# Optimization experiments

Hardware: AMD Instinct MI355X
Metric: run time of the kernel (lower is better)

The kernel has to match this reference:

```python
import jax, jax.numpy as jnp
import numpy as np

N_NODES = 100000
N_EDGES = 1600000
IN_DIM, HID_DIM, OUT_DIM = 128, 64, 16
BN_EPS = 1e-5


def sage_conv(x, edge_index, W_l, b_l, W_r):
    # PyG SAGEConv (aggr='mean'): out = lin_l(mean_j x_j) + lin_r(x_i)
    src, dst = edge_index[0], edge_index[1]
    msgs = x[src]                                   # [E, F] gather
    sums = jax.ops.segment_sum(msgs, dst, num_segments=N_NODES)      # [N, F]
    cnt = jax.ops.segment_sum(jnp.ones((src.shape[0],), x.dtype), dst,
                              num_segments=N_NODES)                  # [N]
    agg = sums / jnp.maximum(cnt, 1.0)[:, None]     # mean; 0 for isolated nodes
    return agg @ W_l.T + b_l + x @ W_r.T


def batchnorm(x, gamma, beta):
    # BatchNorm1d in training mode: normalize over the node (batch) axis
    mean = jnp.mean(x, axis=0)
    var = jnp.var(x, axis=0)
    return (x - mean) * jax.lax.rsqrt(var + BN_EPS) * gamma + beta


def setup_inputs() -> dict:
    key = jax.random.key(0)
    ks = jax.random.split(key, 8)
    x = jax.random.normal(ks[0], (N_NODES, IN_DIM), dtype=jnp.float32)
    edge_index = jax.random.randint(ks[1], (2, N_EDGES), 0, N_NODES)
    s1 = 1.0 / np.sqrt(IN_DIM)
    s2 = 1.0 / np.sqrt(HID_DIM)
    return {
        "x": x,
        "edge_index": edge_index,
        "W1_l": jax.random.uniform(ks[2], (HID_DIM, IN_DIM), minval=-s1, maxval=s1),
        "b1": jnp.zeros((HID_DIM,), jnp.float32),
        "W1_r": jax.random.uniform(ks[3], (HID_DIM, IN_DIM), minval=-s1, maxval=s1),
        "bn_gamma": jnp.ones((HID_DIM,), jnp.float32),
        "bn_beta": jnp.zeros((HID_DIM,), jnp.float32),
        "W2_l": jax.random.uniform(ks[4], (OUT_DIM, HID_DIM), minval=-s2, maxval=s2),
        "b2": jnp.zeros((OUT_DIM,), jnp.float32),
        "W2_r": jax.random.uniform(ks[5], (OUT_DIM, HID_DIM), minval=-s2, maxval=s2),
    }


def reference(x, edge_index, W1_l, b1, W1_r, bn_gamma, bn_beta, W2_l, b2, W2_r):
    h = sage_conv(x, edge_index, W1_l, b1, W1_r)
    h = jax.nn.relu(batchnorm(h, bn_gamma, bn_beta))
    return sage_conv(h, edge_index, W2_l, b2, W2_r)
```

## Files before the change

kernel.cpp:

```cpp
#include <hip/hip_runtime.h>

#define NN 100000
#define NE 1600000
#define NPB 128
#define NBK 782
#define EPB 16384
#define NPART 98
#define NTILES 1563
#define CAP 4096

#define OFF_H      0
#define OFF_YL     6400000
#define OFF_YR     9600000
#define OFF_EBUF   12800000
#define OFF_HIST   14400000
#define OFF_BSTART 14500000
#define OFF_BCURP  14500800
#define OFF_BCNTP  14513312
#define OFF_BNACC  14525824

typedef __attribute__((ext_vector_type(8))) short bf16x8;
typedef __attribute__((ext_vector_type(4))) float f32x4;

__device__ __forceinline__ ushort f2bf(float f) {
  unsigned u = __float_as_uint(f);
  u += 0x7fffu + ((u >> 16) & 1);
  return (ushort)(u >> 16);
}
#define BFLO(u) __uint_as_float(((u) & 0xffffu) << 16)
#define BFHI(u) __uint_as_float((u) & 0xffff0000u)

__global__ __launch_bounds__(1024) void k_bcnt2(const int* __restrict__ ei,
                                                int* __restrict__ bcntp) {
  __shared__ int cnt[NBK];
  const int tid = threadIdx.x;
  for (int i = tid; i < NBK; i += 1024) cnt[i] = 0;
  __syncthreads();
  const int per = (NE + gridDim.x - 1) / gridDim.x;
  int e0 = blockIdx.x * per;
  int e1 = min(e0 + per, NE);
  for (int e = e0 + tid; e < e1; e += 1024)
    atomicAdd(&cnt[ei[NE + e] >> 7], 1);
  __syncthreads();
  for (int b = tid; b < NBK; b += 1024)
    if (cnt[b]) atomicAdd(&bcntp[b * 16], cnt[b]);
}

__global__ __launch_bounds__(1024) void k_bprep(const int* __restrict__ bcntp,
                                                int* __restrict__ bstart,
                                                int* __restrict__ bcurp) {
  __shared__ int sd[1024];
  int t = threadIdx.x;
  int v = (t < NBK) ? bcntp[t * 16] : 0;
  sd[t] = v;
  __syncthreads();
  for (int off = 1; off < 1024; off <<= 1) {
    int u = (t >= off) ? sd[t - off] : 0;
    __syncthreads();
    sd[t] += u;
    __syncthreads();
  }
  if (t < NBK) { int s = sd[t] - v; bstart[t] = s; bcurp[t * 16] = s; }
  if (t == 0) bstart[NBK] = NE;
}

__global__ __launch_bounds__(512) void k_pg(const int* __restrict__ ei,
                                            int* __restrict__ bcurp,
                                            int* __restrict__ ebuf,
                                            const float* __restrict__ x,
                                            const float* __restrict__ W1l,
                                            const float* __restrict__ W1r,
                                            ushort* __restrict__ yl,
                                            ushort* __restrict__ yr) {
  __shared__ ushort smem[64 * 136 + 128 * 136];
  const int tid = threadIdx.x;

  if (blockIdx.x < NPART) {
    int* cnt = (int*)smem;
    int* gstart = cnt + NBK;
    int* cur = gstart + NBK;
    int e0 = blockIdx.x * EPB;
    int e1 = min(e0 + EPB, NE);
    for (int i = tid; i < NBK; i += 512) cnt[i] = 0;
    __syncthreads();
    for (int e = e0 + tid; e < e1; e += 512)
      atomicAdd(&cnt[ei[NE + e] >> 7], 1);
    __syncthreads();
    for (int b = tid; b < NBK; b += 512) {
      int c = cnt[b];
      gstart[b] = c ? atomicAdd(&bcurp[b * 16], c) : 0;
      cur[b] = 0;
    }
    __syncthreads();
    for (int e = e0 + tid; e < e1; e += 512) {
      int s = ei[e], t = ei[NE + e];
      int b = t >> 7;
      int r = atomicAdd(&cur[b], 1);
      ebuf[gstart[b] + r] = (s << 7) | (t & 127);
    }
    return;
  }

  ushort* xs = smem;
  ushort* wss = smem + 64 * 136;
  const int n0 = (blockIdx.x - NPART) * 64;

  for (int i = tid; i < 64 * 32; i += 512) {
    int r = i >> 5, c = i & 31;
    int n = n0 + r;
    float4 v = (n < NN) ? *(const float4*)&x[(size_t)n * 128 + c * 4]
                        : make_float4(0.f, 0.f, 0.f, 0.f);
    *(ushort4*)&xs[r * 136 + c * 4] = make_ushort4(f2bf(v.x), f2bf(v.y), f2bf(v.z), f2bf(v.w));
  }
  for (int i = tid; i < 128 * 32; i += 512) {
    int r = i >> 5, c = i & 31;
    const float* src = (r < 64) ? &W1l[r * 128 + c * 4] : &W1r[(r - 64) * 128 + c * 4];
    float4 v = *(const float4*)src;
    *(ushort4*)&wss[r * 136 + c * 4] = make_ushort4(f2bf(v.x), f2bf(v.y), f2bf(v.z), f2bf(v.w));
  }
  __syncthreads();

  const int w = tid >> 6, l = tid & 63;
  const int col = l & 15, kb = l >> 4;

  f32x4 acc[4];
#pragma unroll
  for (int nt = 0; nt < 4; ++nt) acc[nt] = (f32x4){0.f, 0.f, 0.f, 0.f};

#pragma unroll
  for (int kc = 0; kc < 4; ++kc) {
    int koff = kc * 32 + kb * 8;
    bf16x8 a[4];
#pragma unroll
    for (int nt = 0; nt < 4; ++nt)
      a[nt] = *(const bf16x8*)&xs[(nt * 16 + col) * 136 + koff];
    bf16x8 b = *(const bf16x8*)&wss[(w * 16 + col) * 136 + koff];
#pragma unroll
    for (int nt = 0; nt < 4; ++nt)
      acc[nt] = __builtin_amdgcn_mfma_f32_16x16x32_bf16(a[nt], b, acc[nt], 0, 0, 0);
  }

  const int outc = w * 16 + col;
#pragma unroll
  for (int nt = 0; nt < 4; ++nt) {
#pragma unroll
    for (int r = 0; r < 4; ++r) {
      int n = n0 + nt * 16 + kb * 4 + r;
      if (n < NN) {
        ushort v = f2bf(acc[nt][r]);
        if (outc < 64) yl[(size_t)n * 64 + outc] = v;
        else           yr[(size_t)n * 64 + (outc - 64)] = v;
      }
    }
  }
}

__global__ __launch_bounds__(512) void k_agg1c(int* __restrict__ ebuf,
                                               const int* __restrict__ bstart,
                                               int* __restrict__ hist,
                                               const ushort* __restrict__ yl,
                                               const ushort* __restrict__ yr,
                                               const float* __restrict__ b1,
                                               float* __restrict__ h,
                                               float* __restrict__ bnacc) {
  __shared__ int raw[CAP];
  __shared__ int srt[CAP];
  __shared__ int sd[128], deg[128], offx[128], cursor[128];
  __shared__ float bnWs[8][64], bnWq[8][64];
  const int tid = threadIdx.x;
  const int b = blockIdx.x;
  const int node0 = b << 7;
  const int nnode = min(NPB, NN - node0);
  const int kstart = bstart[b];
  const int T = min(bstart[b + 1] - kstart, CAP);

  if (tid < 128) deg[tid] = 0;
  __syncthreads();
  for (int i = tid; i < T; i += 512) {
    int e = ebuf[kstart + i];
    raw[i] = e;
    atomicAdd(&deg[e & 127], 1);
  }
  __syncthreads();
  if (tid < 128) sd[tid] = deg[tid];
  __syncthreads();
  for (int o = 1; o < 128; o <<= 1) {
    int v = (tid < 128 && tid >= o) ? sd[tid - o] : 0;
    __syncthreads();
    if (tid < 128) sd[tid] += v;
    __syncthreads();
  }
  if (tid < 128) {
    int s = sd[tid] - deg[tid];
    offx[tid] = s;
    cursor[tid] = s;
    if (tid < nnode) hist[node0 + tid] = deg[tid];
  }
  __syncthreads();

  for (int i = tid; i < T; i += 512) {
    int e = raw[i];
    int slot = atomicAdd(&cursor[e & 127], 1);
    srt[slot] = e >> 7;
  }
  __syncthreads();

  for (int i = tid; i < T; i += 512) ebuf[kstart + i] = srt[i];

  const int g = tid >> 3, f8 = tid & 7;
  float s[8] = {}, q[8] = {};
#pragma unroll
  for (int rep = 0; rep < 2; ++rep) {
    int dl = g + rep * 64;
    if (dl < nnode) {
      int st = offx[dl], d = deg[dl];
      float a[8] = {};
      int k = st, ke = st + d;
      for (; k + 3 < ke; k += 4) {
        int s0 = srt[k], s1 = srt[k + 1], s2 = srt[k + 2], s3 = srt[k + 3];
        uint4 v0 = *(const uint4*)&yl[(size_t)s0 * 64 + f8 * 8];
        uint4 v1 = *(const uint4*)&yl[(size_t)s1 * 64 + f8 * 8];
        uint4 v2 = *(const uint4*)&yl[(size_t)s2 * 64 + f8 * 8];
        uint4 v3 = *(const uint4*)&yl[(size_t)s3 * 64 + f8 * 8];
        a[0] += (BFLO(v0.x) + BFLO(v1.x)) + (BFLO(v2.x) + BFLO(v3.x));
        a[1] += (BFHI(v0.x) + BFHI(v1.x)) + (BFHI(v2.x) + BFHI(v3.x));
        a[2] += (BFLO(v0.y) + BFLO(v1.y)) + (BFLO(v2.y) + BFLO(v3.y));
        a[3] += (BFHI(v0.y) + BFHI(v1.y)) + (BFHI(v2.y) + BFHI(v3.y));
        a[4] += (BFLO(v0.z) + BFLO(v1.z)) + (BFLO(v2.z) + BFLO(v3.z));
        a[5] += (BFHI(v0.z) + BFHI(v1.z)) + (BFHI(v2.z) + BFHI(v3.z));
        a[6] += (BFLO(v0.w) + BFLO(v1.w)) + (BFLO(v2.w) + BFLO(v3.w));
        a[7] += (BFHI(v0.w) + BFHI(v1.w)) + (BFHI(v2.w) + BFHI(v3.w));
      }
      for (; k < ke; ++k) {
        int s0 = srt[k];
        uint4 v0 = *(const uint4*)&yl[(size_t)s0 * 64 + f8 * 8];
        a[0] += BFLO(v0.x); a[1] += BFHI(v0.x);
        a[2] += BFLO(v0.y); a[3] += BFHI(v0.y);
        a[4] += BFLO(v0.z); a[5] += BFHI(v0.z);
        a[6] += BFLO(v0.w); a[7] += BFHI(v0.w);
      }
      int node = node0 + dl;
      float invc = 1.0f / fmaxf((float)d, 1.0f);
      uint4 rv = *(const uint4*)&yr[(size_t)node * 64 + f8 * 8];
      float4 bv0 = *(const float4*)&b1[f8 * 8];
      float4 bv1 = *(const float4*)&b1[f8 * 8 + 4];
      float hv[8];
      hv[0] = a[0] * invc + bv0.x + BFLO(rv.x);
      hv[1] = a[1] * invc + bv0.y + BFHI(rv.x);
      hv[2] = a[2] * invc + bv0.z + BFLO(rv.y);
      hv[3] = a[3] * invc + bv0.w + BFHI(rv.y);
      hv[4] = a[4] * invc + bv1.x + BFLO(rv.z);
      hv[5] = a[5] * invc + bv1.y + BFHI(rv.z);
      hv[6] = a[6] * invc + bv1.z + BFLO(rv.w);
      hv[7] = a[7] * invc + bv1.w + BFHI(rv.w);
      *(float4*)&h[(size_t)node * 64 + f8 * 8]     = make_float4(hv[0], hv[1], hv[2], hv[3]);
      *(float4*)&h[(size_t)node * 64 + f8 * 8 + 4] = make_float4(hv[4], hv[5], hv[6], hv[7]);
#pragma unroll
      for (int j = 0; j < 8; ++j) { s[j] += hv[j]; q[j] += hv[j] * hv[j]; }
    }
  }

#pragma unroll
  for (int j = 0; j < 8; ++j) {
    s[j] += __shfl_xor(s[j], 8);  s[j] += __shfl_xor(s[j], 16); s[j] += __shfl_xor(s[j], 32);
    q[j] += __shfl_xor(q[j], 8);  q[j] += __shfl_xor(q[j], 16); q[j] += __shfl_xor(q[j], 32);
  }
  const int w = tid >> 6, lane = tid & 63;
  if (lane < 8) {
#pragma unroll
    for (int j = 0; j < 8; ++j) {
      bnWs[w][lane * 8 + j] = s[j];
      bnWq[w][lane * 8 + j] = q[j];
    }
  }
  __syncthreads();
  if (tid < 64) {
    float S = 0.f, Q = 0.f;
#pragma unroll
    for (int ww = 0; ww < 8; ++ww) { S += bnWs[ww][tid]; Q += bnWq[ww][tid]; }
    atomicAdd(&bnacc[tid], S);
    atomicAdd(&bnacc[64 + tid], Q);
  }
}

__global__ __launch_bounds__(256) void k_layer2m(const float* __restrict__ h,
                                                 const float* __restrict__ W2l,
                                                 const float* __restrict__ W2r,
                                                 const float* __restrict__ b2,
                                                 const float* __restrict__ bnacc,
                                                 const float* __restrict__ gamma,
                                                 const float* __restrict__ beta,
                                                 ushort* __restrict__ zl,
                                                 float* __restrict__ zr) {
  __shared__ ushort hs[64 * 72];
  __shared__ ushort wss[32 * 72];
  __shared__ float sc[64], sh[64];
  const int tid = threadIdx.x;
  const int n0 = blockIdx.x * 64;

  if (tid < 64) {
    float mean = bnacc[tid] * (1.0f / NN);
    float var = bnacc[64 + tid] * (1.0f / NN) - mean * mean;
    float scv = gamma[tid] * rsqrtf(var + 1e-5f);
    sc[tid] = scv;
    sh[tid] = beta[tid] - mean * scv;
  }
  for (int i = tid; i < 32 * 16; i += 256) {
    int r = i >> 4, c = i & 15;
    const float* src = (r < 16) ? &W2l[r * 64 + c * 4] : &W2r[(r - 16) * 64 + c * 4];
    float4 v = *(const float4*)src;
    *(ushort4*)&wss[r * 72 + c * 4] = make_ushort4(f2bf(v.x), f2bf(v.y), f2bf(v.z), f2bf(v.w));
  }
  __syncthreads();

  for (int i = tid; i < 64 * 16; i += 256) {
    int r = i >> 4, c = i & 15;
    int n = n0 + r;
    float4 v = (n < NN) ? *(const float4*)&h[(size_t)n * 64 + c * 4]
                        : make_float4(0.f, 0.f, 0.f, 0.f);
    float4 o;
    o.x = fmaxf(v.x * sc[c * 4 + 0] + sh[c * 4 + 0], 0.f);
    o.y = fmaxf(v.y * sc[c * 4 + 1] + sh[c * 4 + 1], 0.f);
    o.z = fmaxf(v.z * sc[c * 4 + 2] + sh[c * 4 + 2], 0.f);
    o.w = fmaxf(v.w * sc[c * 4 + 3] + sh[c * 4 + 3], 0.f);
    *(ushort4*)&hs[r * 72 + c * 4] = make_ushort4(f2bf(o.x), f2bf(o.y), f2bf(o.z), f2bf(o.w));
  }
  __syncthreads();

  const int w = tid >> 6, l = tid & 63;
  const int col = l & 15, kb = l >> 4;

  f32x4 acc[2] = {(f32x4){0.f, 0.f, 0.f, 0.f}, (f32x4){0.f, 0.f, 0.f, 0.f}};
#pragma unroll
  for (int kc = 0; kc < 2; ++kc) {
    int koff = kc * 32 + kb * 8;
    bf16x8 a = *(const bf16x8*)&hs[(w * 16 + col) * 72 + koff];
    bf16x8 b0 = *(const bf16x8*)&wss[col * 72 + koff];
    bf16x8 b1v = *(const bf16x8*)&wss[(16 + col) * 72 + koff];
    acc[0] = __builtin_amdgcn_mfma_f32_16x16x32_bf16(a, b0, acc[0], 0, 0, 0);
    acc[1] = __builtin_amdgcn_mfma_f32_16x16x32_bf16(a, b1v, acc[1], 0, 0, 0);
  }

#pragma unroll
  for (int r = 0; r < 4; ++r) {
    int n = n0 + w * 16 + kb * 4 + r;
    if (n < NN) {
      zl[(size_t)n * 16 + col] = f2bf(acc[0][r]);
      zr[(size_t)n * 16 + col] = acc[1][r] + b2[col];
    }
  }
}

__global__ __launch_bounds__(512) void k_agg2c(const int* __restrict__ ebuf,
                                               const int* __restrict__ bstart,
                                               const int* __restrict__ hist,
                                               const ushort* __restrict__ zl,
                                               const float* __restrict__ zr,
                                               float* __restrict__ out) {
  __shared__ int elist[CAP];
  __shared__ int sd[128], deg[128], offx[128];
  const int tid = threadIdx.x;
  const int b = blockIdx.x;
  const int node0 = b << 7;
  const int nnode = min(NPB, NN - node0);
  const int kstart = bstart[b];
  const int T = min(bstart[b + 1] - kstart, CAP);

  for (int i = tid; i < T; i += 512) elist[i] = ebuf[kstart + i];
  if (tid < 128) {
    int d = (tid < nnode) ? hist[node0 + tid] : 0;
    deg[tid] = d;
    sd[tid] = d;
  }
  __syncthreads();
  for (int o = 1; o < 128; o <<= 1) {
    int v = (tid < 128 && tid >= o) ? sd[tid - o] : 0;
    __syncthreads();
    if (tid < 128) sd[tid] += v;
    __syncthreads();
  }
  if (tid < 128) offx[tid] = sd[tid] - deg[tid];
  __syncthreads();

  const int g = tid >> 3, f8 = tid & 7;
#pragma unroll
  for (int rep = 0; rep < 2; ++rep) {
    int dl = g + rep * 64;
    if (dl < nnode) {
      int st = offx[dl], d = deg[dl];
      float a0 = 0.f, a1 = 0.f;
      int k = st, ke = st + d;
      for (; k + 3 < ke; k += 4) {
        int s0 = elist[k], s1 = elist[k + 1], s2 = elist[k + 2], s3 = elist[k + 3];
        unsigned v0 = *(const unsigned*)&zl[(size_t)s0 * 16 + f8 * 2];
        unsigned v1 = *(const unsigned*)&zl[(size_t)s1 * 16 + f8 * 2];
        unsigned v2 = *(const unsigned*)&zl[(size_t)s2 * 16 + f8 * 2];
        unsigned v3 = *(const unsigned*)&zl[(size_t)s3 * 16 + f8 * 2];
        a0 += (BFLO(v0) + BFLO(v1)) + (BFLO(v2) + BFLO(v3));
        a1 += (BFHI(v0) + BFHI(v1)) + (BFHI(v2) + BFHI(v3));
      }
      for (; k < ke; ++k) {
        unsigned v0 = *(const unsigned*)&zl[(size_t)elist[k] * 16 + f8 * 2];
        a0 += BFLO(v0);
        a1 += BFHI(v0);
      }
      int node = node0 + dl;
      float invc = 1.0f / fmaxf((float)d, 1.0f);
      size_t base = (size_t)node * 16 + f8 * 2;
      out[base]     = a0 * invc + zr[base];
      out[base + 1] = a1 * invc + zr[base + 1];
    }
  }
}

extern "C" void kernel_launch(void* const* d_in, const int* in_sizes, int n_in,
                              void* d_out, int out_size, void* d_ws, size_t ws_size,
                              hipStream_t stream) {
  const float* x     = (const float*)d_in[0];
  const int*   ei    = (const int*)d_in[1];
  const float* W1l   = (const float*)d_in[2];
  const float* b1    = (const float*)d_in[3];
  const float* W1r   = (const float*)d_in[4];
  const float* gamma = (const float*)d_in[5];
  const float* beta  = (const float*)d_in[6];
  const float* W2l   = (const float*)d_in[7];
  const float* b2    = (const float*)d_in[8];
  const float* W2r   = (const float*)d_in[9];
  float* out = (float*)d_out;
  float* ws  = (float*)d_ws;

  float*  hbuf   = ws + OFF_H;
  ushort* yl     = (ushort*)(ws + OFF_YL);
  ushort* yr     = (ushort*)(ws + OFF_YR);
  ushort* zl     = (ushort*)(ws + OFF_YL);
  float*  zr     = ws + OFF_YR;
  int*    ebuf   = (int*)(ws + OFF_EBUF);
  int*    hist   = (int*)(ws + OFF_HIST);
  int*    bstart = (int*)(ws + OFF_BSTART);
  int*    bcurp  = (int*)(ws + OFF_BCURP);
  int*    bcntp  = (int*)(ws + OFF_BCNTP);
  float*  bnacc  = ws + OFF_BNACC;

  hipMemsetAsync(bcntp, 0, (12512 + 128) * sizeof(int), stream);

  k_bcnt2<<<98, 1024, 0, stream>>>(ei, bcntp);
  k_bprep<<<1, 1024, 0, stream>>>(bcntp, bstart, bcurp);
  k_pg<<<NPART + NTILES, 512, 0, stream>>>(ei, bcurp, ebuf, x, W1l, W1r, yl, yr);
  k_agg1c<<<NBK, 512, 0, stream>>>(ebuf, bstart, hist, yl, yr, b1, hbuf, bnacc);
  k_layer2m<<<NTILES, 256, 0, stream>>>(hbuf, W2l, W2r, b2, bnacc, gamma, beta, zl, zr);
  k_agg2c<<<NBK, 512, 0, stream>>>(ebuf, bstart, hist, zl, zr, out);
}
```

Baseline: 138.0 us.

## Precompute per-block bucket offsets and pre-convert weights to bf16 once

The bucket count kernel now writes per-partition histograms, and the prefix kernel computes a fixed offset for every partition and bucket. The scatter blocks therefore skip recounting destinations and the global atomic cursor reservation. Weight fp32-to-bf16 conversion moves into extra blocks of the count kernel, so the GEMM tiles read bf16 weights straight from global memory instead of each block converting them into LDS. The trade-off is a serial 98-step loop per thread in the single-block prefix kernel, and weight fragment loads in the MFMA loops that now come from global or cache rather than LDS.

```diff
diff --git a/kernel.cpp b/kernel.cpp
--- a/kernel.cpp
+++ b/kernel.cpp
@@ -6,18 +6,21 @@
 #define NBK 782
 #define EPB 16384
 #define NPART 98
+#define NCVT 18
 #define NTILES 1563
 #define CAP 4096
 
 #define OFF_H      0
+#define OFF_GCNT   0
+#define OFF_GOFS   80000
+#define OFF_W1BF   160000
 #define OFF_YL     6400000
 #define OFF_YR     9600000
 #define OFF_EBUF   12800000
 #define OFF_HIST   14400000
 #define OFF_BSTART 14500000
-#define OFF_BCURP  14500800
-#define OFF_BCNTP  14513312
-#define OFF_BNACC  14525824
+#define OFF_BNACC  14500800
+#define OFF_W2BF   14500928
 
 typedef __attribute__((ext_vector_type(8))) short bf16x8;
 typedef __attribute__((ext_vector_type(4))) float f32x4;
@@ -31,28 +34,45 @@
 #define BFHI(u) __uint_as_float((u) & 0xffff0000u)
 
 __global__ __launch_bounds__(1024) void k_bcnt2(const int* __restrict__ ei,
-                                                int* __restrict__ bcntp) {
+                                                int* __restrict__ gcnt,
+                                                const float* __restrict__ W1l,
+                                                const float* __restrict__ W1r,
+                                                const float* __restrict__ W2l,
+                                                const float* __restrict__ W2r,
+                                                ushort* __restrict__ w1bf,
+                                                ushort* __restrict__ w2bf) {
+  const int tid = threadIdx.x;
+  if (blockIdx.x >= NPART) {
+    int i = (blockIdx.x - NPART) * 1024 + tid;
+    if (i < 16384) {
+      w1bf[i] = f2bf(i < 8192 ? W1l[i] : W1r[i - 8192]);
+    } else if (i < 16384 + 2048) {
+      int j = i - 16384;
+      w2bf[j] = f2bf(j < 1024 ? W2l[j] : W2r[j - 1024]);
+    }
+    return;
+  }
   __shared__ int cnt[NBK];
-  const int tid = threadIdx.x;
   for (int i = tid; i < NBK; i += 1024) cnt[i] = 0;
   __syncthreads();
-  const int per = (NE + gridDim.x - 1) / gridDim.x;
-  int e0 = blockIdx.x * per;
-  int e1 = min(e0 + per, NE);
+  int e0 = blockIdx.x * EPB;
+  int e1 = min(e0 + EPB, NE);
   for (int e = e0 + tid; e < e1; e += 1024)
     atomicAdd(&cnt[ei[NE + e] >> 7], 1);
   __syncthreads();
   for (int b = tid; b < NBK; b += 1024)
-    if (cnt[b]) atomicAdd(&bcntp[b * 16], cnt[b]);
-}
-
-__global__ __launch_bounds__(1024) void k_bprep(const int* __restrict__ bcntp,
+    gcnt[blockIdx.x * NBK + b] = cnt[b];
+}
+
+__global__ __launch_bounds__(1024) void k_bprep(const int* __restrict__ gcnt,
                                                 int* __restrict__ bstart,
-                                                int* __restrict__ bcurp) {
+                                                int* __restrict__ gofs) {
   __shared__ int sd[1024];
   int t = threadIdx.x;
-  int v = (t < NBK) ? bcntp[t * 16] : 0;
-  sd[t] = v;
+  int total = 0;
+  if (t < NBK)
+    for (int blk = 0; blk < NPART; ++blk) total += gcnt[blk * NBK + t];
+  sd[t] = total;
   __syncthreads();
   for (int off = 1; off < 1024; off <<= 1) {
     int u = (t >= off) ? sd[t - off] : 0;
@@ -60,38 +80,37 @@
     sd[t] += u;
     __syncthreads();
   }
-  if (t < NBK) { int s = sd[t] - v; bstart[t] = s; bcurp[t * 16] = s; }
+  if (t < NBK) {
+    int run = sd[t] - total;
+    bstart[t] = run;
+    for (int blk = 0; blk < NPART; ++blk) {
+      gofs[blk * NBK + t] = run;
+      run += gcnt[blk * NBK + t];
+    }
+  }
   if (t == 0) bstart[NBK] = NE;
 }
 
 __global__ __launch_bounds__(512) void k_pg(const int* __restrict__ ei,
-                                            int* __restrict__ bcurp,
+                                            const int* __restrict__ gofs,
                                             int* __restrict__ ebuf,
                                             const float* __restrict__ x,
-                                            const float* __restrict__ W1l,
-                                            const float* __restrict__ W1r,
+                                            const ushort* __restrict__ w1bf,
                                             ushort* __restrict__ yl,
                                             ushort* __restrict__ yr) {
-  __shared__ ushort smem[64 * 136 + 128 * 136];
+  __shared__ ushort smem[64 * 136];
   const int tid = threadIdx.x;
 
   if (blockIdx.x < NPART) {
-    int* cnt = (int*)smem;
-    int* gstart = cnt + NBK;
+    int* gstart = (int*)smem;
     int* cur = gstart + NBK;
+    for (int i = tid; i < NBK; i += 512) {
+      gstart[i] = gofs[blockIdx.x * NBK + i];
+      cur[i] = 0;
+    }
+    __syncthreads();
     int e0 = blockIdx.x * EPB;
     int e1 = min(e0 + EPB, NE);
-    for (int i = tid; i < NBK; i += 512) cnt[i] = 0;
-    __syncthreads();
-    for (int e = e0 + tid; e < e1; e += 512)
-      atomicAdd(&cnt[ei[NE + e] >> 7], 1);
-    __syncthreads();
-    for (int b = tid; b < NBK; b += 512) {
-      int c = cnt[b];
-      gstart[b] = c ? atomicAdd(&bcurp[b * 16], c) : 0;
-      cur[b] = 0;
-    }
-    __syncthreads();
     for (int e = e0 + tid; e < e1; e += 512) {
       int s = ei[e], t = ei[NE + e];
       int b = t >> 7;
@@ -102,7 +121,6 @@
   }
 
   ushort* xs = smem;
-  ushort* wss = smem + 64 * 136;
   const int n0 = (blockIdx.x - NPART) * 64;
 
   for (int i = tid; i < 64 * 32; i += 512) {
@@ -112,12 +130,6 @@
                         : make_float4(0.f, 0.f, 0.f, 0.f);
     *(ushort4*)&xs[r * 136 + c * 4] = make_ushort4(f2bf(v.x), f2bf(v.y), f2bf(v.z), f2bf(v.w));
   }
-  for (int i = tid; i < 128 * 32; i += 512) {
-    int r = i >> 5, c = i & 31;
-    const float* src = (r < 64) ? &W1l[r * 128 + c * 4] : &W1r[(r - 64) * 128 + c * 4];
-    float4 v = *(const float4*)src;
-    *(ushort4*)&wss[r * 136 + c * 4] = make_ushort4(f2bf(v.x), f2bf(v.y), f2bf(v.z), f2bf(v.w));
-  }
   __syncthreads();
 
   const int w = tid >> 6, l = tid & 63;
@@ -134,7 +146,7 @@
 #pragma unroll
     for (int nt = 0; nt < 4; ++nt)
       a[nt] = *(const bf16x8*)&xs[(nt * 16 + col) * 136 + koff];
-    bf16x8 b = *(const bf16x8*)&wss[(w * 16 + col) * 136 + koff];
+    bf16x8 b = *(const bf16x8*)&w1bf[(w * 16 + col) * 128 + koff];
 #pragma unroll
     for (int nt = 0; nt < 4; ++nt)
       acc[nt] = __builtin_amdgcn_mfma_f32_16x16x32_bf16(a[nt], b, acc[nt], 0, 0, 0);
@@ -284,8 +296,7 @@
 }
 
 __global__ __launch_bounds__(256) void k_layer2m(const float* __restrict__ h,
-                                                 const float* __restrict__ W2l,
-                                                 const float* __restrict__ W2r,
+                                                 const ushort* __restrict__ w2bf,
                                                  const float* __restrict__ b2,
                                                  const float* __restrict__ bnacc,
                                                  const float* __restrict__ gamma,
@@ -293,7 +304,6 @@
                                                  ushort* __restrict__ zl,
                                                  float* __restrict__ zr) {
   __shared__ ushort hs[64 * 72];
-  __shared__ ushort wss[32 * 72];
   __shared__ float sc[64], sh[64];
   const int tid = threadIdx.x;
   const int n0 = blockIdx.x * 64;
@@ -304,12 +314,6 @@
     float scv = gamma[tid] * rsqrtf(var + 1e-5f);
     sc[tid] = scv;
     sh[tid] = beta[tid] - mean * scv;
-  }
-  for (int i = tid; i < 32 * 16; i += 256) {
-    int r = i >> 4, c = i & 15;
-    const float* src = (r < 16) ? &W2l[r * 64 + c * 4] : &W2r[(r - 16) * 64 + c * 4];
-    float4 v = *(const float4*)src;
-    *(ushort4*)&wss[r * 72 + c * 4] = make_ushort4(f2bf(v.x), f2bf(v.y), f2bf(v.z), f2bf(v.w));
   }
   __syncthreads();
 
@@ -335,8 +339,8 @@
   for (int kc = 0; kc < 2; ++kc) {
     int koff = kc * 32 + kb * 8;
     bf16x8 a = *(const bf16x8*)&hs[(w * 16 + col) * 72 + koff];
-    bf16x8 b0 = *(const bf16x8*)&wss[col * 72 + koff];
-    bf16x8 b1v = *(const bf16x8*)&wss[(16 + col) * 72 + koff];
+    bf16x8 b0 = *(const bf16x8*)&w2bf[col * 64 + koff];
+    bf16x8 b1v = *(const bf16x8*)&w2bf[(16 + col) * 64 + koff];
     acc[0] = __builtin_amdgcn_mfma_f32_16x16x32_bf16(a, b0, acc[0], 0, 0, 0);
     acc[1] = __builtin_amdgcn_mfma_f32_16x16x32_bf16(a, b1v, acc[1], 0, 0, 0);
   }
@@ -430,6 +434,9 @@
   float* ws  = (float*)d_ws;
 
   float*  hbuf   = ws + OFF_H;
+  int*    gcnt   = (int*)(ws + OFF_GCNT);
+  int*    gofs   = (int*)(ws + OFF_GOFS);
+  ushort* w1bf   = (ushort*)(ws + OFF_W1BF);
   ushort* yl     = (ushort*)(ws + OFF_YL);
   ushort* yr     = (ushort*)(ws + OFF_YR);
   ushort* zl     = (ushort*)(ws + OFF_YL);
@@ -437,16 +444,15 @@
   int*    ebuf   = (int*)(ws + OFF_EBUF);
   int*    hist   = (int*)(ws + OFF_HIST);
   int*    bstart = (int*)(ws + OFF_BSTART);
-  int*    bcurp  = (int*)(ws + OFF_BCURP);
-  int*    bcntp  = (int*)(ws + OFF_BCNTP);
   float*  bnacc  = ws + OFF_BNACC;
-
-  hipMemsetAsync(bcntp, 0, (12512 + 128) * sizeof(int), stream);
-
-  k_bcnt2<<<98, 1024, 0, stream>>>(ei, bcntp);
-  k_bprep<<<1, 1024, 0, stream>>>(bcntp, bstart, bcurp);
-  k_pg<<<NPART + NTILES, 512, 0, stream>>>(ei, bcurp, ebuf, x, W1l, W1r, yl, yr);
+  ushort* w2bf   = (ushort*)(ws + OFF_W2BF);
+
+  hipMemsetAsync(bnacc, 0, 128 * sizeof(float), stream);
+
+  k_bcnt2<<<NPART + NCVT, 1024, 0, stream>>>(ei, gcnt, W1l, W1r, W2l, W2r, w1bf, w2bf);
+  k_bprep<<<1, 1024, 0, stream>>>(gcnt, bstart, gofs);
+  k_pg<<<NPART + NTILES, 512, 0, stream>>>(ei, gofs, ebuf, x, w1bf, yl, yr);
   k_agg1c<<<NBK, 512, 0, stream>>>(ebuf, bstart, hist, yl, yr, b1, hbuf, bnacc);
-  k_layer2m<<<NTILES, 256, 0, stream>>>(hbuf, W2l, W2r, b2, bnacc, gamma, beta, zl, zr);
+  k_layer2m<<<NTILES, 256, 0, stream>>>(hbuf, w2bf, b2, bnacc, gamma, beta, zl, zr);
   k_agg2c<<<NBK, 512, 0, stream>>>(ebuf, bstart, hist, zl, zr, out);
 }
```

After: 139.5 us. No clear change (+1.1%).
